# Performance work log

Hardware: AMD Instinct MI355X
Metric: run time of the kernel (lower is better)

The kernel has to match this reference:

```python
import jax, jax.numpy as jnp
import numpy as np

N = 200000
C_IN, C_OUT = 32, 64
D, H, W = 32, 512, 512
EPS = 1e-5


def _build_nbrs(lin, d, h, w, offsets):
    # lin: sorted unique linear voxel indices [N]; returns [N, K] int64 (sentinel=N)
    n = lin.shape[0]
    cols = []
    for dz, dy, dx in offsets:
        nd, nh, nw = d + dz, h + dy, w + dx
        valid = (nd >= 0) & (nd < D) & (nh >= 0) & (nh < H) & (nw >= 0) & (nw < W)
        nlin = nd * (H * W) + nh * W + nw
        pos = np.searchsorted(lin, nlin)
        posc = np.clip(pos, 0, n - 1)
        found = valid & (pos < n) & (lin[posc] == nlin)
        cols.append(np.where(found, posc, n))
    return np.stack(cols, axis=1).astype(np.int64)


def setup_inputs() -> dict:
    rng = np.random.default_rng(0)
    lin = np.sort(rng.choice(D * H * W, size=N, replace=False))
    d = lin // (H * W)
    h = (lin // W) % H
    w = lin % W
    # (1,3,3) kernel, padding (0,1,1): dz=0
    off133 = [(0, dy, dx) for dy in (-1, 0, 1) for dx in (-1, 0, 1)]
    # (3,1,3) kernel, padding (1,0,1): dy=0
    off313 = [(dz, 0, dx) for dz in (-1, 0, 1) for dx in (-1, 0, 1)]
    nbr133 = jnp.asarray(_build_nbrs(lin, d, h, w, off133))
    nbr313 = jnp.asarray(_build_nbrs(lin, d, h, w, off313))

    key = jax.random.key(0)
    ks = jax.random.split(key, 5)
    feats = jax.random.normal(ks[0], (N, C_IN), dtype=jnp.float32)
    s_in = 1.0 / np.sqrt(9 * C_IN)
    s_out = 1.0 / np.sqrt(9 * C_OUT)
    W1 = jax.random.normal(ks[1], (9, C_IN, C_OUT), dtype=jnp.float32) * s_in
    W2 = jax.random.normal(ks[2], (9, C_OUT, C_OUT), dtype=jnp.float32) * s_out
    W3 = jax.random.normal(ks[3], (9, C_IN, C_OUT), dtype=jnp.float32) * s_in
    W4 = jax.random.normal(ks[4], (9, C_OUT, C_OUT), dtype=jnp.float32) * s_out
    ones = jnp.ones((C_OUT,), jnp.float32)
    zeros = jnp.zeros((C_OUT,), jnp.float32)
    return dict(feats=feats, nbr133=nbr133, nbr313=nbr313,
                W1=W1, W2=W2, W3=W3, W4=W4,
                g0=ones, b0=zeros, g02=ones, b02=zeros,
                g1=ones, b1=zeros, g2=ones, b2=zeros)


def _subm_conv(x, nbr, Wk):
    # x: [N, Cin], nbr: [N, K] with sentinel N -> zero row, Wk: [K, Cin, Cout]
    xp = jnp.concatenate([x, jnp.zeros((1, x.shape[1]), x.dtype)], axis=0)
    g = xp[nbr]  # [N, K, Cin] gather
    return jnp.einsum('nkc,kcd->nd', g, Wk)


def _bn(x, gamma, beta):
    # training-mode BatchNorm1d: batch stats over N (biased variance)
    m = x.mean(axis=0)
    v = x.var(axis=0)
    return gamma * (x - m) * jax.lax.rsqrt(v + EPS) + beta


def _lrelu(x):
    return jax.nn.leaky_relu(x, 0.01)


def reference(feats, nbr133, nbr313, W1, W2, W3, W4,
              g0, b0, g02, b02, g1, b1, g2, b2):
    shortcut = _subm_conv(feats, nbr133, W1)
    shortcut = _bn(_lrelu(shortcut), g0, b0)
    shortcut = _subm_conv(shortcut, nbr313, W2)
    shortcut = _bn(_lrelu(shortcut), g02, b02)

    resA = _subm_conv(feats, nbr313, W3)
    resA = _bn(_lrelu(resA), g1, b1)
    resA = _subm_conv(resA, nbr133, W4)
    resA = _bn(_lrelu(resA), g2, b2)
    return resA + shortcut
```

## Files before the change

kernel.cpp:

```cpp
#include <hip/hip_runtime.h>
#include <hip/hip_bf16.h>


typedef __attribute__((ext_vector_type(8))) short bf16x8;
typedef __attribute__((ext_vector_type(4))) float f32x4;
typedef unsigned long long ull;

#define EPSF 1e-5f
#define REP8 0x0101010101010101ull

__device__ __forceinline__ unsigned short f2bf(float f) {
    union { __hip_bfloat16 h; unsigned short u; } cv;
    cv.h = __float2bfloat16(f);
    return cv.u;
}
__device__ __forceinline__ unsigned pkbf(float lo, float hi) {
    return (unsigned)f2bf(lo) | ((unsigned)f2bf(hi) << 16);
}

__global__ void prep_kernel(const float* __restrict__ W1, const float* __restrict__ W3,
                            unsigned short* __restrict__ Wb1, unsigned short* __restrict__ Wb3)
{
    int i = blockIdx.x * 256 + threadIdx.x;
    if (i >= 2 * 9 * 2048) return;
    const float* W = i < 9 * 2048 ? W1 : W3;
    unsigned short* Wb = i < 9 * 2048 ? Wb1 : Wb3;
    int pp = i < 9 * 2048 ? i : i - 9 * 2048;
    int k = pp >> 11, rest = pp & 2047;
    int t = (rest >> 9) & 3, lane = (rest >> 3) & 63, j = rest & 7;
    int c = (lane >> 4) * 8 + j;
    int d = t * 16 + (lane & 15);
    Wb[pp] = f2bf(W[(size_t)(k * 32 + c) * 64 + d]);
}

__global__ __launch_bounds__(256, 4)
void conv13_kernel(const float* __restrict__ x,
                   const int* __restrict__ nbrA, const int* __restrict__ nbrB,
                   const unsigned short* __restrict__ WbA,
                   const unsigned short* __restrict__ WbB,
                   unsigned short* __restrict__ yA, unsigned short* __restrict__ yB,
                   float* __restrict__ part,
                   int n_vox)
{
    const int lane = threadIdx.x & 63;
    const int wave = threadIdx.x >> 6;
    __shared__ __align__(16) char smem[4][4352];
    char* my = smem[wave];
    const int c15 = lane & 15, g16 = lane >> 4;
    const int j7 = lane & 7, kk = j7 + (j7 >= 4 ? 1 : 0), vv = lane >> 3;
    const int v16 = blockIdx.x * 64 + wave * 16;

    const size_t r0 = (size_t)(v16 + vv) * 9 + kk;
    const size_t r1 = (size_t)(v16 + 8 + vv) * 9 + kk;
    int pA0 = nbrA[r0], pA1 = nbrA[r1];
    int pB0 = nbrB[r0], pB1 = nbrB[r1];

    const float* xr = x + (size_t)(v16 + c15) * 32 + g16 * 8;
    float4 x0 = *reinterpret_cast<const float4*>(xr);
    float4 x1 = *reinterpret_cast<const float4*>(xr + 4);

    bf16x8 bA[4], bB[4];
    #pragma unroll
    for (int t = 0; t < 4; ++t) {
        bA[t] = *reinterpret_cast<const bf16x8*>(WbA + (size_t)((4*4+t)*64 + lane) * 8);
        bB[t] = *reinterpret_cast<const bf16x8*>(WbB + (size_t)((4*4+t)*64 + lane) * 8);
    }
    bf16x8 af;
    af[0]=(short)f2bf(x0.x); af[1]=(short)f2bf(x0.y); af[2]=(short)f2bf(x0.z); af[3]=(short)f2bf(x0.w);
    af[4]=(short)f2bf(x1.x); af[5]=(short)f2bf(x1.y); af[6]=(short)f2bf(x1.z); af[7]=(short)f2bf(x1.w);

    f32x4 accA[4], accB[4];
    #pragma unroll
    for (int t = 0; t < 4; ++t) { f32x4 z = {0.f,0.f,0.f,0.f}; accA[t] = z; accB[t] = z; }
    #pragma unroll
    for (int t = 0; t < 4; ++t) {
        accA[t] = __builtin_amdgcn_mfma_f32_16x16x32_bf16(af, bA[t], accA[t], 0, 0, 0);
        accB[t] = __builtin_amdgcn_mfma_f32_16x16x32_bf16(af, bB[t], accB[t], 0, 0, 0);
    }

    ull mA0 = __ballot(pA0 < n_vox), mA1 = __ballot(pA1 < n_vox);
    ull mB0 = __ballot(pB0 < n_vox), mB1 = __ballot(pB1 < n_vox);
    const int nhA = __popcll(mA0) + __popcll(mA1);
    const int nhB = __popcll(mB0) + __popcll(mB1);

    auto walksel = [&](ull M, int preg, int slot, int base, int& sel) {
        while (M) {
            int b = __builtin_ctzll(M); M &= M - 1;
            int src = __shfl(preg, b);
            sel = (c15 == slot - base) ? src : sel;
            ++slot;
        }
        return slot;
    };
    auto gatherfrag = [&](int sel) {
        const float* hr = x + (size_t)sel * 32 + g16 * 8;
        float4 f0 = *reinterpret_cast<const float4*>(hr);
        float4 f1 = *reinterpret_cast<const float4*>(hr + 4);
        bf16x8 h;
        h[0]=(short)f2bf(f0.x); h[1]=(short)f2bf(f0.y); h[2]=(short)f2bf(f0.z); h[3]=(short)f2bf(f0.w);
        h[4]=(short)f2bf(f1.x); h[5]=(short)f2bf(f1.y); h[6]=(short)f2bf(f1.z); h[7]=(short)f2bf(f1.w);
        return h;
    };
    auto kloop = [&](ull m0, ull m1, bf16x8 h, const unsigned short* Wb,
                     f32x4* acc, int base) {
        const int pref = __popcll(m0);
        for (int tap = 0; tap < 8; ++tap) {
            ull TM = REP8 << tap;
            ull k0 = m0 & TM, k1 = m1 & TM;
            if (!(k0 | k1)) continue;
            int k = tap + (tap >= 4 ? 1 : 0);
            bf16x8 bk[4];
            #pragma unroll
            for (int t = 0; t < 4; ++t)
                bk[t] = *reinterpret_cast<const bf16x8*>(Wb + (size_t)((k*4+t)*64 + lane) * 8);
            f32x4 ch[4];
            #pragma unroll
            for (int t = 0; t < 4; ++t) { f32x4 z = {0.f,0.f,0.f,0.f}; ch[t] = z; }
            #pragma unroll
            for (int t = 0; t < 4; ++t)
                ch[t] = __builtin_amdgcn_mfma_f32_16x16x32_bf16(h, bk[t], ch[t], 0, 0, 0);
            auto inj = [&](ull M, ull msrc, int spref, int vbase) {
                while (M) {
                    int b = __builtin_ctzll(M); M &= M - 1;
                    int slot = spref + __popcll(msrc & ((1ull << b) - 1ull));
                    int rs = slot - base;
                    if (rs < 0 || rs >= 16) continue;
                    int vb = vbase + (b >> 3);
                    int srclane = ((rs >> 2) << 4) + c15;
                    int jj = rs & 3, gp = vb >> 2, jp = vb & 3;
                    float v0, v1, v2, v3;
                    switch (jj) {
                    case 0: v0=__shfl(ch[0][0],srclane); v1=__shfl(ch[1][0],srclane);
                            v2=__shfl(ch[2][0],srclane); v3=__shfl(ch[3][0],srclane); break;
                    case 1: v0=__shfl(ch[0][1],srclane); v1=__shfl(ch[1][1],srclane);
                            v2=__shfl(ch[2][1],srclane); v3=__shfl(ch[3][1],srclane); break;
                    case 2: v0=__shfl(ch[0][2],srclane); v1=__shfl(ch[1][2],srclane);
                            v2=__shfl(ch[2][2],srclane); v3=__shfl(ch[3][2],srclane); break;
                    default: v0=__shfl(ch[0][3],srclane); v1=__shfl(ch[1][3],srclane);
                             v2=__shfl(ch[2][3],srclane); v3=__shfl(ch[3][3],srclane); break;
                    }
                    bool mine = (g16 == gp);
                    float z0 = mine ? v0 : 0.f, z1 = mine ? v1 : 0.f;
                    float z2 = mine ? v2 : 0.f, z3 = mine ? v3 : 0.f;
                    switch (jp) {
                    case 0: acc[0][0]+=z0; acc[1][0]+=z1; acc[2][0]+=z2; acc[3][0]+=z3; break;
                    case 1: acc[0][1]+=z0; acc[1][1]+=z1; acc[2][1]+=z2; acc[3][1]+=z3; break;
                    case 2: acc[0][2]+=z0; acc[1][2]+=z1; acc[2][2]+=z2; acc[3][2]+=z3; break;
                    default: acc[0][3]+=z0; acc[1][3]+=z1; acc[2][3]+=z2; acc[3][3]+=z3; break;
                    }
                }
            };
            inj(k0, m0, 0, 0);
            inj(k1, m1, pref, 8);
        }
    };

    if (nhA | nhB) {
        int selA = 0, selB = 0;
        int cA = walksel(mA0, pA0, 0, 0, selA);
        walksel(mA1, pA1, cA, 0, selA);
        int cB = walksel(mB0, pB0, 0, 0, selB);
        walksel(mB1, pB1, cB, 0, selB);
        bf16x8 hA = gatherfrag(selA);
        bf16x8 hB = gatherfrag(selB);
        if (nhA) kloop(mA0, mA1, hA, WbA, accA, 0);
        if (nhB) kloop(mB0, mB1, hB, WbB, accB, 0);
        for (int base = 16; base < nhA; base += 16) {
            int s = 0;
            int c0 = walksel(mA0, pA0, 0, base, s);
            walksel(mA1, pA1, c0, base, s);
            kloop(mA0, mA1, gatherfrag(s), WbA, accA, base);
        }
        for (int base = 16; base < nhB; base += 16) {
            int s = 0;
            int c0 = walksel(mB0, pB0, 0, base, s);
            walksel(mB1, pB1, c0, base, s);
            kloop(mB0, mB1, gatherfrag(s), WbB, accB, base);
        }
    }

    float psA0[4], psA1[4], psB0[4], psB1[4];
    #pragma unroll
    for (int t = 0; t < 4; ++t) { psA0[t]=0.f; psA1[t]=0.f; psB0[t]=0.f; psB1[t]=0.f; }

    auto epi = [&](f32x4* acc, float* ps0, float* ps1, unsigned short* yo) {
        float* stg = reinterpret_cast<float*>(my);
        #pragma unroll
        for (int t = 0; t < 4; ++t) {
            const int col = t * 16 + c15;
            #pragma unroll
            for (int j = 0; j < 4; ++j) {
                float v = acc[t][j];
                v = v > 0.f ? v : 0.01f * v;
                ps0[t] += v;
                ps1[t] = fmaf(v, v, ps1[t]);
                stg[(g16 * 4 + j) * 68 + col] = v;
            }
        }
        const int mm = lane >> 2, cc0 = (lane & 3) * 16;
        float4 q0 = *reinterpret_cast<float4*>(&stg[mm * 68 + cc0]);
        float4 q1 = *reinterpret_cast<float4*>(&stg[mm * 68 + cc0 + 4]);
        float4 q2 = *reinterpret_cast<float4*>(&stg[mm * 68 + cc0 + 8]);
        float4 q3 = *reinterpret_cast<float4*>(&stg[mm * 68 + cc0 + 12]);
        uint4 o0, o1;
        o0.x = pkbf(q0.x, q0.y); o0.y = pkbf(q0.z, q0.w);
        o0.z = pkbf(q1.x, q1.y); o0.w = pkbf(q1.z, q1.w);
        o1.x = pkbf(q2.x, q2.y); o1.y = pkbf(q2.z, q2.w);
        o1.z = pkbf(q3.x, q3.y); o1.w = pkbf(q3.z, q3.w);
        uint4* dst = reinterpret_cast<uint4*>(yo + (size_t)(v16 + mm) * 64 + cc0);
        dst[0] = o0; dst[1] = o1;
    };
    epi(accA, psA0, psA1, yA);
    epi(accB, psB0, psB1, yB);

    __syncthreads();
    float* lsf = reinterpret_cast<float*>(&smem[0][0]);
    const int r = wave * 4 + g16;
    #pragma unroll
    for (int t = 0; t < 4; ++t) {
        lsf[r * 256 + 0 * 64 + t * 16 + c15] = psA0[t];
        lsf[r * 256 + 1 * 64 + t * 16 + c15] = psA1[t];
        lsf[r * 256 + 2 * 64 + t * 16 + c15] = psB0[t];
        lsf[r * 256 + 3 * 64 + t * 16 + c15] = psB1[t];
    }
    __syncthreads();
    const int tid = threadIdx.x;
    float s = 0.f;
    #pragma unroll
    for (int rr = 0; rr < 16; ++rr) s += lsf[rr * 256 + tid];
    part[(size_t)blockIdx.x * 256 + tid] = s;
}

__global__ __launch_bounds__(256, 4)
void conv24_kernel(const unsigned short* __restrict__ x2, const int* __restrict__ nbr2,
                   const float* __restrict__ tv2, const unsigned short* __restrict__ Wb2,
                   unsigned short* __restrict__ y2,
                   const unsigned short* __restrict__ x4, const int* __restrict__ nbr4,
                   const float* __restrict__ tv4, const unsigned short* __restrict__ Wb4,
                   unsigned short* __restrict__ y4,
                   float* __restrict__ part,
                   int n_vox, int ntile)
{
    const int lane = threadIdx.x & 63;
    const int wave = threadIdx.x >> 6;
    __shared__ __align__(16) char smem[4][4352];
    char* my = smem[wave];
    const bool second = blockIdx.x >= ntile;
    const int tile = second ? blockIdx.x - ntile : blockIdx.x;
    const unsigned short* x = second ? x4 : x2;
    const int* nbr = second ? nbr4 : nbr2;
    const float* tvec = second ? tv4 : tv2;
    const unsigned short* Wb = second ? Wb4 : Wb2;
    unsigned short* yout = second ? y4 : y2;

    const int c15 = lane & 15, g16 = lane >> 4;
    const int j7 = lane & 7, kk = j7 + (j7 >= 4 ? 1 : 0), vv = lane >> 3;
    const int v16 = tile * 64 + wave * 16;

    const size_t r0 = (size_t)(v16 + vv) * 9 + kk;
    const size_t r1 = (size_t)(v16 + 8 + vv) * 9 + kk;
    int p0 = nbr[r0], p1 = nbr[r1];

    const unsigned short* xr = x + (size_t)(v16 + c15) * 64 + g16 * 8;
    bf16x8 a0 = *reinterpret_cast<const bf16x8*>(xr);
    bf16x8 a1 = *reinterpret_cast<const bf16x8*>(xr + 32);

    bf16x8 bwC[2][4];
    #pragma unroll
    for (int kt = 0; kt < 2; ++kt)
        #pragma unroll
        for (int t = 0; t < 4; ++t)
            bwC[kt][t] = *reinterpret_cast<const bf16x8*>(Wb + (size_t)(((4*2+kt)*4+t)*64 + lane) * 8);

    f32x4 acc[4];
    #pragma unroll
    for (int t = 0; t < 4; ++t) {
        float tC = tvec[4 * 64 + t * 16 + c15];
        f32x4 z = {tC, tC, tC, tC};
        acc[t] = z;
    }
    #pragma unroll
    for (int t = 0; t < 4; ++t) {
        acc[t] = __builtin_amdgcn_mfma_f32_16x16x32_bf16(a0, bwC[0][t], acc[t], 0, 0, 0);
        acc[t] = __builtin_amdgcn_mfma_f32_16x16x32_bf16(a1, bwC[1][t], acc[t], 0, 0, 0);
    }

    ull m0 = __ballot(p0 < n_vox), m1 = __ballot(p1 < n_vox);
    const int nh = __popcll(m0) + __popcll(m1);

    auto walksel = [&](ull M, int preg, int slot, int base, int& sel) {
        while (M) {
            int b = __builtin_ctzll(M); M &= M - 1;
            int src = __shfl(preg, b);
            sel = (c15 == slot - base) ? src : sel;
            ++slot;
        }
        return slot;
    };
    auto kloop = [&](bf16x8 h0, bf16x8 h1, int base) {
        const int pref = __popcll(m0);
        for (int tap = 0; tap < 8; ++tap) {
            ull TM = REP8 << tap;
            ull k0 = m0 & TM, k1 = m1 & TM;
            if (!(k0 | k1)) continue;
            int k = tap + (tap >= 4 ? 1 : 0);
            bf16x8 bk[2][4];
            #pragma unroll
            for (int kt = 0; kt < 2; ++kt)
                #pragma unroll
                for (int t = 0; t < 4; ++t)
                    bk[kt][t] = *reinterpret_cast<const bf16x8*>(Wb + (size_t)(((k*2+kt)*4+t)*64 + lane) * 8);
            float tvk[4];
            #pragma unroll
            for (int t = 0; t < 4; ++t) tvk[t] = tvec[k * 64 + t * 16 + c15];
            f32x4 ch[4];
            #pragma unroll
            for (int t = 0; t < 4; ++t) { f32x4 z = {0.f,0.f,0.f,0.f}; ch[t] = z; }
            #pragma unroll
            for (int t = 0; t < 4; ++t) {
                ch[t] = __builtin_amdgcn_mfma_f32_16x16x32_bf16(h0, bk[0][t], ch[t], 0, 0, 0);
                ch[t] = __builtin_amdgcn_mfma_f32_16x16x32_bf16(h1, bk[1][t], ch[t], 0, 0, 0);
            }
            auto inj = [&](ull M, ull msrc, int spref, int vbase) {
                while (M) {
                    int b = __builtin_ctzll(M); M &= M - 1;
                    int slot = spref + __popcll(msrc & ((1ull << b) - 1ull));
                    int rs = slot - base;
                    if (rs < 0 || rs >= 16) continue;
                    int vb = vbase + (b >> 3);
                    int srclane = ((rs >> 2) << 4) + c15;
                    int jj = rs & 3, gp = vb >> 2, jp = vb & 3;
                    float v0, v1, v2, v3;
                    switch (jj) {
                    case 0: v0=__shfl(ch[0][0],srclane); v1=__shfl(ch[1][0],srclane);
                            v2=__shfl(ch[2][0],srclane); v3=__shfl(ch[3][0],srclane); break;
                    case 1: v0=__shfl(ch[0][1],srclane); v1=__shfl(ch[1][1],srclane);
                            v2=__shfl(ch[2][1],srclane); v3=__shfl(ch[3][1],srclane); break;
                    case 2: v0=__shfl(ch[0][2],srclane); v1=__shfl(ch[1][2],srclane);
                            v2=__shfl(ch[2][2],srclane); v3=__shfl(ch[3][2],srclane); break;
                    default: v0=__shfl(ch[0][3],srclane); v1=__shfl(ch[1][3],srclane);
                             v2=__shfl(ch[2][3],srclane); v3=__shfl(ch[3][3],srclane); break;
                    }
                    bool mine = (g16 == gp);
                    float z0 = mine ? (v0 + tvk[0]) : 0.f, z1 = mine ? (v1 + tvk[1]) : 0.f;
                    float z2 = mine ? (v2 + tvk[2]) : 0.f, z3 = mine ? (v3 + tvk[3]) : 0.f;
                    switch (jp) {
                    case 0: acc[0][0]+=z0; acc[1][0]+=z1; acc[2][0]+=z2; acc[3][0]+=z3; break;
                    case 1: acc[0][1]+=z0; acc[1][1]+=z1; acc[2][1]+=z2; acc[3][1]+=z3; break;
                    case 2: acc[0][2]+=z0; acc[1][2]+=z1; acc[2][2]+=z2; acc[3][2]+=z3; break;
                    default: acc[0][3]+=z0; acc[1][3]+=z1; acc[2][3]+=z2; acc[3][3]+=z3; break;
                    }
                }
            };
            inj(k0, m0, 0, 0);
            inj(k1, m1, pref, 8);
        }
    };

    for (int base = 0; base < nh; base += 16) {
        int sel = 0;
        int c0 = walksel(m0, p0, 0, base, sel);
        walksel(m1, p1, c0, base, sel);
        const unsigned short* hr = x + (size_t)sel * 64 + g16 * 8;
        bf16x8 h0 = *reinterpret_cast<const bf16x8*>(hr);
        bf16x8 h1 = *reinterpret_cast<const bf16x8*>(hr + 32);
        kloop(h0, h1, base);
    }

    float ps0[4] = {0,0,0,0}, ps1[4] = {0,0,0,0};
    float* stg = reinterpret_cast<float*>(my);
    #pragma unroll
    for (int t = 0; t < 4; ++t) {
        const int col = t * 16 + c15;
        #pragma unroll
        for (int j = 0; j < 4; ++j) {
            float v = acc[t][j];
            v = v > 0.f ? v : 0.01f * v;
            ps0[t] += v;
            ps1[t] = fmaf(v, v, ps1[t]);
            stg[(g16 * 4 + j) * 68 + col] = v;
        }
    }
    const int mm = lane >> 2, cc0 = (lane & 3) * 16;
    float4 q0 = *reinterpret_cast<float4*>(&stg[mm * 68 + cc0]);
    float4 q1 = *reinterpret_cast<float4*>(&stg[mm * 68 + cc0 + 4]);
    float4 q2 = *reinterpret_cast<float4*>(&stg[mm * 68 + cc0 + 8]);
    float4 q3 = *reinterpret_cast<float4*>(&stg[mm * 68 + cc0 + 12]);
    uint4 o0, o1;
    o0.x = pkbf(q0.x, q0.y); o0.y = pkbf(q0.z, q0.w);
    o0.z = pkbf(q1.x, q1.y); o0.w = pkbf(q1.z, q1.w);
    o1.x = pkbf(q2.x, q2.y); o1.y = pkbf(q2.z, q2.w);
    o1.z = pkbf(q3.x, q3.y); o1.w = pkbf(q3.z, q3.w);
    uint4* dst = reinterpret_cast<uint4*>(yout + (size_t)(v16 + mm) * 64 + cc0);
    dst[0] = o0; dst[1] = o1;

    __syncthreads();
    float* lsf = reinterpret_cast<float*>(&smem[0][0]);
    const int r = wave * 4 + g16;
    #pragma unroll
    for (int t = 0; t < 4; ++t) {
        lsf[r * 128 + t * 16 + c15] = ps0[t];
        lsf[r * 128 + 64 + t * 16 + c15] = ps1[t];
    }
    __syncthreads();
    const int tid = threadIdx.x;
    if (tid < 128) {
        float s = 0.f;
        #pragma unroll
        for (int rr = 0; rr < 16; ++rr) s += lsf[rr * 128 + tid];
        part[(size_t)tile * 256 + (second ? 128 : 0) + tid] = s;
    }
}

__global__ void bnred_kernel(const float* __restrict__ part,
                             const float* __restrict__ gA, const float* __restrict__ bA,
                             const float* __restrict__ gB, const float* __restrict__ bB,
                             float* __restrict__ scA, float* __restrict__ shA,
                             float* __restrict__ scB, float* __restrict__ shB,
                             float invN, int nblk)
{
    const int l = blockIdx.x >> 6, c = blockIdx.x & 63;
    const float* base = part + (size_t)(l * 2) * 64 + c;
    __shared__ float red[256][2];
    float s = 0.f, q = 0.f;
    for (int b = threadIdx.x; b < nblk; b += 256) {
        s += base[(size_t)b * 256];
        q += base[(size_t)b * 256 + 64];
    }
    red[threadIdx.x][0] = s; red[threadIdx.x][1] = q;
    __syncthreads();
    for (int off = 128; off; off >>= 1) {
        if (threadIdx.x < off) {
            red[threadIdx.x][0] += red[threadIdx.x + off][0];
            red[threadIdx.x][1] += red[threadIdx.x + off][1];
        }
        __syncthreads();
    }
    if (threadIdx.x == 0) {
        float m = red[0][0] * invN;
        float v = red[0][1] * invN - m * m;
        const float* g = l ? gB : gA;
        const float* bb = l ? bB : bA;
        float* sc = l ? scB : scA;
        float* sh = l ? shB : shA;
        float scale = g[c] / sqrtf(v + EPSF);
        sc[c] = scale;
        sh[c] = bb[c] - m * scale;
    }
}

__global__ void foldpack_kernel(const float* __restrict__ W2, const float* __restrict__ W4,
                                const float* __restrict__ sc1, const float* __restrict__ sh1,
                                const float* __restrict__ sc3, const float* __restrict__ sh3,
                                float* __restrict__ t2, float* __restrict__ t4,
                                unsigned short* __restrict__ Wb2, unsigned short* __restrict__ Wb4)
{
    int i = blockIdx.x * 256 + threadIdx.x;
    if (i < 2 * 9 * 64) {
        const float* W = i < 9 * 64 ? W2 : W4;
        const float* shift = i < 9 * 64 ? sh1 : sh3;
        float* tv = i < 9 * 64 ? t2 : t4;
        int ii = i < 9 * 64 ? i : i - 9 * 64;
        int d = ii & 63, k = ii >> 6;
        float t = 0.f;
        for (int c = 0; c < 64; ++c)
            t = fmaf(shift[c], W[((size_t)k * 64 + c) * 64 + d], t);
        tv[ii] = t;
    } else {
        int p = i - 2 * 9 * 64;
        if (p >= 2 * 9 * 4096) return;
        const float* W = p < 9 * 4096 ? W2 : W4;
        const float* scale = p < 9 * 4096 ? sc1 : sc3;
        unsigned short* Wb = p < 9 * 4096 ? Wb2 : Wb4;
        int pp = p < 9 * 4096 ? p : p - 9 * 4096;
        int k = pp >> 12, rest = pp & 4095;
        int kt = rest >> 11, t = (rest >> 9) & 3, lane = (rest >> 3) & 63, j = rest & 7;
        int c = kt * 32 + (lane >> 4) * 8 + j;
        int d = t * 16 + (lane & 15);
        Wb[pp] = f2bf(scale[c] * W[((size_t)k * 64 + c) * 64 + d]);
    }
}

__global__ void final_kernel(const unsigned short* __restrict__ y2,
                             const unsigned short* __restrict__ y4,
                             const float* __restrict__ sc2, const float* __restrict__ sh2,
                             const float* __restrict__ sc4, const float* __restrict__ sh4,
                             float* __restrict__ out, int n8)
{
    int i = blockIdx.x * 256 + threadIdx.x;
    if (i >= n8) return;
    const int c0 = (i & 7) * 8;
    uint4 aq = *reinterpret_cast<const uint4*>(y2 + (size_t)i * 8);
    uint4 bq = *reinterpret_cast<const uint4*>(y4 + (size_t)i * 8);
    float a[8], b[8];
    a[0] = __uint_as_float(aq.x << 16); a[1] = __uint_as_float(aq.x & 0xffff0000u);
    a[2] = __uint_as_float(aq.y << 16); a[3] = __uint_as_float(aq.y & 0xffff0000u);
    a[4] = __uint_as_float(aq.z << 16); a[5] = __uint_as_float(aq.z & 0xffff0000u);
    a[6] = __uint_as_float(aq.w << 16); a[7] = __uint_as_float(aq.w & 0xffff0000u);
    b[0] = __uint_as_float(bq.x << 16); b[1] = __uint_as_float(bq.x & 0xffff0000u);
    b[2] = __uint_as_float(bq.y << 16); b[3] = __uint_as_float(bq.y & 0xffff0000u);
    b[4] = __uint_as_float(bq.z << 16); b[5] = __uint_as_float(bq.z & 0xffff0000u);
    b[6] = __uint_as_float(bq.w << 16); b[7] = __uint_as_float(bq.w & 0xffff0000u);
    float r[8];
    #pragma unroll
    for (int j = 0; j < 8; ++j)
        r[j] = fmaf(a[j], sc2[c0 + j], sh2[c0 + j]) + fmaf(b[j], sc4[c0 + j], sh4[c0 + j]);
    float4 o0 = {r[0], r[1], r[2], r[3]};
    float4 o1 = {r[4], r[5], r[6], r[7]};
    float* po = out + (size_t)i * 8;
    *reinterpret_cast<float4*>(po) = o0;
    *reinterpret_cast<float4*>(po + 4) = o1;
}

extern "C" void kernel_launch(void* const* d_in, const int* in_sizes, int n_in,
                              void* d_out, int out_size, void* d_ws, size_t ws_size,
                              hipStream_t stream)
{
    const float* feats  = (const float*)d_in[0];
    const int*   nbr133 = (const int*)d_in[1];
    const int*   nbr313 = (const int*)d_in[2];
    const float* W1 = (const float*)d_in[3];
    const float* W2 = (const float*)d_in[4];
    const float* W3 = (const float*)d_in[5];
    const float* W4 = (const float*)d_in[6];
    const float* g0  = (const float*)d_in[7];
    const float* b0  = (const float*)d_in[8];
    const float* g02 = (const float*)d_in[9];
    const float* b02 = (const float*)d_in[10];
    const float* g1  = (const float*)d_in[11];
    const float* b1  = (const float*)d_in[12];
    const float* g2  = (const float*)d_in[13];
    const float* b2  = (const float*)d_in[14];

    const int N = in_sizes[0] / 32;
    const int ntile = N >> 6;

    char* w = (char*)d_ws;
    auto alloc = [&](size_t bytes) {
        char* p = w;
        w += (bytes + 255) & ~(size_t)255;
        return p;
    };
    unsigned short* y1 = (unsigned short*)alloc((size_t)N * 64 * 2);
    unsigned short* y3 = (unsigned short*)alloc((size_t)N * 64 * 2);
    unsigned short* y2 = (unsigned short*)alloc((size_t)N * 64 * 2);
    unsigned short* y4 = (unsigned short*)alloc((size_t)N * 64 * 2);
    float* t2 = (float*)alloc(9 * 64 * 4);
    float* t4 = (float*)alloc(9 * 64 * 4);
    unsigned short* Wb1 = (unsigned short*)alloc(9 * 4 * 64 * 8 * 2);
    unsigned short* Wb3 = (unsigned short*)alloc(9 * 4 * 64 * 8 * 2);
    unsigned short* Wb2 = (unsigned short*)alloc(9 * 2 * 4 * 64 * 8 * 2);
    unsigned short* Wb4 = (unsigned short*)alloc(9 * 2 * 4 * 64 * 8 * 2);
    float* part13 = (float*)alloc((size_t)ntile * 256 * 4);
    float* part24 = (float*)alloc((size_t)ntile * 256 * 4);
    float* scl = (float*)alloc(8 * 64 * 4);
    float *sc1 = scl,       *sh1 = scl + 64;
    float *sc3 = scl + 128, *sh3 = scl + 192;
    float *sc2 = scl + 256, *sh2 = scl + 320;
    float *sc4 = scl + 384, *sh4 = scl + 448;

    const float invN = 1.0f / (float)N;

    prep_kernel<<<(2 * 9 * 2048 + 255) / 256, 256, 0, stream>>>(W1, W3, Wb1, Wb3);

    conv13_kernel<<<ntile, 256, 0, stream>>>(feats, nbr133, nbr313, Wb1, Wb3,
                                             y1, y3, part13, N);
    bnred_kernel<<<128, 256, 0, stream>>>(part13, g0, b0, g1, b1,
                                          sc1, sh1, sc3, sh3, invN, ntile);
    foldpack_kernel<<<(2 * 9 * 64 + 2 * 9 * 4096 + 255) / 256, 256, 0, stream>>>(
        W2, W4, sc1, sh1, sc3, sh3, t2, t4, Wb2, Wb4);

    conv24_kernel<<<2 * ntile, 256, 0, stream>>>(y1, nbr313, t2, Wb2, y2,
                                                 y3, nbr133, t4, Wb4, y4,
                                                 part24, N, ntile);
    bnred_kernel<<<128, 256, 0, stream>>>(part24, g02, b02, g2, b2,
                                          sc2, sh2, sc4, sh4, invN, ntile);

    final_kernel<<<(N * 8 + 255) / 256, 256, 0, stream>>>(
        y2, y4, sc2, sh2, sc4, sh4, (float*)d_out, N * 8);
}
```

Baseline: 131.2 us.

## Process two voxel tiles per block in conv24 to reuse center-tap weights

Each conv24 block now handles two consecutive 64-voxel tiles instead of one. The center-tap weights are loaded once and shared, and the center MFMAs for both tiles are interleaved, which halves the block count and amortizes per-block setup and the partial-sum reduction. The per-tap weight loads inside the neighbor loop are still repeated for each tile. Extra accumulators raise register pressure, so launch bounds drop to 3 blocks per SM, and the BN partial count passed to the reduction changes accordingly.

```diff
diff --git a/kernel.cpp b/kernel.cpp
--- a/kernel.cpp
+++ b/kernel.cpp
@@ -231,7 +231,7 @@
     part[(size_t)blockIdx.x * 256 + tid] = s;
 }
 
-__global__ __launch_bounds__(256, 4)
+__global__ __launch_bounds__(256, 3)
 void conv24_kernel(const unsigned short* __restrict__ x2, const int* __restrict__ nbr2,
                    const float* __restrict__ tv2, const unsigned short* __restrict__ Wb2,
                    unsigned short* __restrict__ y2,
@@ -239,14 +239,14 @@
                    const float* __restrict__ tv4, const unsigned short* __restrict__ Wb4,
                    unsigned short* __restrict__ y4,
                    float* __restrict__ part,
-                   int n_vox, int ntile)
+                   int n_vox, int ntile, int nb2)
 {
     const int lane = threadIdx.x & 63;
     const int wave = threadIdx.x >> 6;
     __shared__ __align__(16) char smem[4][4352];
     char* my = smem[wave];
-    const bool second = blockIdx.x >= ntile;
-    const int tile = second ? blockIdx.x - ntile : blockIdx.x;
+    const bool second = blockIdx.x >= nb2;
+    const int q = second ? blockIdx.x - nb2 : blockIdx.x;
     const unsigned short* x = second ? x4 : x2;
     const int* nbr = second ? nbr4 : nbr2;
     const float* tvec = second ? tv4 : tv2;
@@ -255,15 +255,28 @@
 
     const int c15 = lane & 15, g16 = lane >> 4;
     const int j7 = lane & 7, kk = j7 + (j7 >= 4 ? 1 : 0), vv = lane >> 3;
-    const int v16 = tile * 64 + wave * 16;
-
-    const size_t r0 = (size_t)(v16 + vv) * 9 + kk;
-    const size_t r1 = (size_t)(v16 + 8 + vv) * 9 + kk;
-    int p0 = nbr[r0], p1 = nbr[r1];
-
-    const unsigned short* xr = x + (size_t)(v16 + c15) * 64 + g16 * 8;
-    bf16x8 a0 = *reinterpret_cast<const bf16x8*>(xr);
-    bf16x8 a1 = *reinterpret_cast<const bf16x8*>(xr + 32);
+    const int t0 = q * 2, t1 = q * 2 + 1;
+    const bool valid1 = t1 < ntile;
+    const int v16a = t0 * 64 + wave * 16;
+    const int v16b = t1 * 64 + wave * 16;
+
+    int pa0 = nbr[(size_t)(v16a + vv) * 9 + kk];
+    int pa1 = nbr[(size_t)(v16a + 8 + vv) * 9 + kk];
+    int pb0 = n_vox, pb1 = n_vox;
+    if (valid1) {
+        pb0 = nbr[(size_t)(v16b + vv) * 9 + kk];
+        pb1 = nbr[(size_t)(v16b + 8 + vv) * 9 + kk];
+    }
+
+    const unsigned short* xra = x + (size_t)(v16a + c15) * 64 + g16 * 8;
+    bf16x8 a0a = *reinterpret_cast<const bf16x8*>(xra);
+    bf16x8 a1a = *reinterpret_cast<const bf16x8*>(xra + 32);
+    bf16x8 a0b = a0a, a1b = a1a;
+    if (valid1) {
+        const unsigned short* xrb = x + (size_t)(v16b + c15) * 64 + g16 * 8;
+        a0b = *reinterpret_cast<const bf16x8*>(xrb);
+        a1b = *reinterpret_cast<const bf16x8*>(xrb + 32);
+    }
 
     bf16x8 bwC[2][4];
     #pragma unroll
@@ -272,21 +285,25 @@
         for (int t = 0; t < 4; ++t)
             bwC[kt][t] = *reinterpret_cast<const bf16x8*>(Wb + (size_t)(((4*2+kt)*4+t)*64 + lane) * 8);
 
-    f32x4 acc[4];
+    f32x4 accA[4], accB[4];
     #pragma unroll
     for (int t = 0; t < 4; ++t) {
         float tC = tvec[4 * 64 + t * 16 + c15];
         f32x4 z = {tC, tC, tC, tC};
-        acc[t] = z;
+        accA[t] = z; accB[t] = z;
     }
     #pragma unroll
     for (int t = 0; t < 4; ++t) {
-        acc[t] = __builtin_amdgcn_mfma_f32_16x16x32_bf16(a0, bwC[0][t], acc[t], 0, 0, 0);
-        acc[t] = __builtin_amdgcn_mfma_f32_16x16x32_bf16(a1, bwC[1][t], acc[t], 0, 0, 0);
-    }
-
-    ull m0 = __ballot(p0 < n_vox), m1 = __ballot(p1 < n_vox);
-    const int nh = __popcll(m0) + __popcll(m1);
+        accA[t] = __builtin_amdgcn_mfma_f32_16x16x32_bf16(a0a, bwC[0][t], accA[t], 0, 0, 0);
+        accB[t] = __builtin_amdgcn_mfma_f32_16x16x32_bf16(a0b, bwC[0][t], accB[t], 0, 0, 0);
+        accA[t] = __builtin_amdgcn_mfma_f32_16x16x32_bf16(a1a, bwC[1][t], accA[t], 0, 0, 0);
+        accB[t] = __builtin_amdgcn_mfma_f32_16x16x32_bf16(a1b, bwC[1][t], accB[t], 0, 0, 0);
+    }
+
+    ull mA0 = __ballot(pa0 < n_vox), mA1 = __ballot(pa1 < n_vox);
+    ull mB0 = __ballot(pb0 < n_vox), mB1 = __ballot(pb1 < n_vox);
+    const int nhA = __popcll(mA0) + __popcll(mA1);
+    const int nhB = __popcll(mB0) + __popcll(mB1);
 
     auto walksel = [&](ull M, int preg, int slot, int base, int& sel) {
         while (M) {
@@ -297,7 +314,7 @@
         }
         return slot;
     };
-    auto kloop = [&](bf16x8 h0, bf16x8 h1, int base) {
+    auto kloop = [&](ull m0, ull m1, bf16x8 h0, bf16x8 h1, f32x4* acc, int base) {
         const int pref = __popcll(m0);
         for (int tap = 0; tap < 8; ++tap) {
             ull TM = REP8 << tap;
@@ -357,42 +374,55 @@
         }
     };
 
-    for (int base = 0; base < nh; base += 16) {
+    for (int base = 0; base < nhA; base += 16) {
         int sel = 0;
-        int c0 = walksel(m0, p0, 0, base, sel);
-        walksel(m1, p1, c0, base, sel);
+        int c0 = walksel(mA0, pa0, 0, base, sel);
+        walksel(mA1, pa1, c0, base, sel);
         const unsigned short* hr = x + (size_t)sel * 64 + g16 * 8;
         bf16x8 h0 = *reinterpret_cast<const bf16x8*>(hr);
         bf16x8 h1 = *reinterpret_cast<const bf16x8*>(hr + 32);
-        kloop(h0, h1, base);
+        kloop(mA0, mA1, h0, h1, accA, base);
+    }
+    for (int base = 0; base < nhB; base += 16) {
+        int sel = 0;
+        int c0 = walksel(mB0, pb0, 0, base, sel);
+        walksel(mB1, pb1, c0, base, sel);
+        const unsigned short* hr = x + (size_t)sel * 64 + g16 * 8;
+        bf16x8 h0 = *reinterpret_cast<const bf16x8*>(hr);
+        bf16x8 h1 = *reinterpret_cast<const bf16x8*>(hr + 32);
+        kloop(mB0, mB1, h0, h1, accB, base);
     }
 
     float ps0[4] = {0,0,0,0}, ps1[4] = {0,0,0,0};
-    float* stg = reinterpret_cast<float*>(my);
-    #pragma unroll
-    for (int t = 0; t < 4; ++t) {
-        const int col = t * 16 + c15;
+    auto epi = [&](f32x4* acc, int v16) {
+        float* stg = reinterpret_cast<float*>(my);
         #pragma unroll
-        for (int j = 0; j < 4; ++j) {
-            float v = acc[t][j];
-            v = v > 0.f ? v : 0.01f * v;
-            ps0[t] += v;
-            ps1[t] = fmaf(v, v, ps1[t]);
-            stg[(g16 * 4 + j) * 68 + col] = v;
-        }
-    }
-    const int mm = lane >> 2, cc0 = (lane & 3) * 16;
-    float4 q0 = *reinterpret_cast<float4*>(&stg[mm * 68 + cc0]);
-    float4 q1 = *reinterpret_cast<float4*>(&stg[mm * 68 + cc0 + 4]);
-    float4 q2 = *reinterpret_cast<float4*>(&stg[mm * 68 + cc0 + 8]);
-    float4 q3 = *reinterpret_cast<float4*>(&stg[mm * 68 + cc0 + 12]);
-    uint4 o0, o1;
-    o0.x = pkbf(q0.x, q0.y); o0.y = pkbf(q0.z, q0.w);
-    o0.z = pkbf(q1.x, q1.y); o0.w = pkbf(q1.z, q1.w);
-    o1.x = pkbf(q2.x, q2.y); o1.y = pkbf(q2.z, q2.w);
-    o1.z = pkbf(q3.x, q3.y); o1.w = pkbf(q3.z, q3.w);
-    uint4* dst = reinterpret_cast<uint4*>(yout + (size_t)(v16 + mm) * 64 + cc0);
-    dst[0] = o0; dst[1] = o1;
+        for (int t = 0; t < 4; ++t) {
+            const int col = t * 16 + c15;
+            #pragma unroll
+            for (int j = 0; j < 4; ++j) {
+                float v = acc[t][j];
+                v = v > 0.f ? v : 0.01f * v;
+                ps0[t] += v;
+                ps1[t] = fmaf(v, v, ps1[t]);
+                stg[(g16 * 4 + j) * 68 + col] = v;
+            }
+        }
+        const int mm = lane >> 2, cc0 = (lane & 3) * 16;
+        float4 q0 = *reinterpret_cast<float4*>(&stg[mm * 68 + cc0]);
+        float4 q1 = *reinterpret_cast<float4*>(&stg[mm * 68 + cc0 + 4]);
+        float4 q2 = *reinterpret_cast<float4*>(&stg[mm * 68 + cc0 + 8]);
+        float4 q3 = *reinterpret_cast<float4*>(&stg[mm * 68 + cc0 + 12]);
+        uint4 o0, o1;
+        o0.x = pkbf(q0.x, q0.y); o0.y = pkbf(q0.z, q0.w);
+        o0.z = pkbf(q1.x, q1.y); o0.w = pkbf(q1.z, q1.w);
+        o1.x = pkbf(q2.x, q2.y); o1.y = pkbf(q2.z, q2.w);
+        o1.z = pkbf(q3.x, q3.y); o1.w = pkbf(q3.z, q3.w);
+        uint4* dst = reinterpret_cast<uint4*>(yout + (size_t)(v16 + mm) * 64 + cc0);
+        dst[0] = o0; dst[1] = o1;
+    };
+    epi(accA, v16a);
+    if (valid1) epi(accB, v16b);
 
     __syncthreads();
     float* lsf = reinterpret_cast<float*>(&smem[0][0]);
@@ -408,7 +438,7 @@
         float s = 0.f;
         #pragma unroll
         for (int rr = 0; rr < 16; ++rr) s += lsf[rr * 128 + tid];
-        part[(size_t)tile * 256 + (second ? 128 : 0) + tid] = s;
+        part[(size_t)q * 256 + (second ? 128 : 0) + tid] = s;
     }
 }
 
@@ -534,6 +564,7 @@
 
     const int N = in_sizes[0] / 32;
     const int ntile = N >> 6;
+    const int nb2 = (ntile + 1) / 2;
 
     char* w = (char*)d_ws;
     auto alloc = [&](size_t bytes) {
@@ -570,11 +601,11 @@
     foldpack_kernel<<<(2 * 9 * 64 + 2 * 9 * 4096 + 255) / 256, 256, 0, stream>>>(
         W2, W4, sc1, sh1, sc3, sh3, t2, t4, Wb2, Wb4);
 
-    conv24_kernel<<<2 * ntile, 256, 0, stream>>>(y1, nbr313, t2, Wb2, y2,
-                                                 y3, nbr133, t4, Wb4, y4,
-                                                 part24, N, ntile);
+    conv24_kernel<<<2 * nb2, 256, 0, stream>>>(y1, nbr313, t2, Wb2, y2,
+                                               y3, nbr133, t4, Wb4, y4,
+                                               part24, N, ntile, nb2);
     bnred_kernel<<<128, 256, 0, stream>>>(part24, g02, b02, g2, b2,
-                                          sc2, sh2, sc4, sh4, invN, ntile);
+                                          sc2, sh2, sc4, sh4, invN, nb2);
 
     final_kernel<<<(N * 8 + 255) / 256, 256, 0, stream>>>(
         y2, y4, sc2, sh2, sc4, sh4, (float*)d_out, N * 8);
```

New measurement: 130.8 us. About the same (-0.3%).
